# Performance work log

Hardware: AMD Instinct MI355X
Metric: run time of the kernel (lower is better)

## Reference

```python
import jax, jax.numpy as jnp
import numpy as np

NQ = 6      # configuration_dim = state_dim // 2
HID = 32    # hidden_dim
NL = 5      # num_layers


def _mlp(x, W0, b0, Wh, bh, Wo, bo):
    # Sequential: NL softplus hidden layers, then linear head
    h = jax.nn.softplus(x @ W0 + b0)
    for i in range(Wh.shape[0]):
        h = jax.nn.softplus(h @ Wh[i] + bh[i])
    return h @ Wo + bo


def _make_mlp_params(key, din, dout):
    k0, k1, k2 = jax.random.split(key, 3)
    s = lambda fan: 1.0 / np.sqrt(fan)
    return (jax.random.normal(k0, (din, HID), jnp.float32) * s(din),
            jnp.zeros((HID,), jnp.float32),
            jax.random.normal(k1, (NL - 1, HID, HID), jnp.float32) * s(HID),
            jnp.zeros((NL - 1, HID), jnp.float32),
            jax.random.normal(k2, (HID, dout), jnp.float32) * s(HID),
            jnp.zeros((dout,), jnp.float32))


def setup_inputs() -> dict:
    key = jax.random.key(0)
    kx, km, ku, kd, ka = jax.random.split(key, 5)
    B, input_dim = 65536, 6
    inputs = jax.random.normal(kx, (B, 2 * NQ + input_dim), jnp.float32)
    m = _make_mlp_params(km, NQ, NQ * NQ)   # mass matrix net
    u = _make_mlp_params(ku, NQ, 1)          # potential energy net
    d = _make_mlp_params(kd, NQ, NQ * NQ)   # damping matrix net
    A = jax.random.normal(ka, (input_dim, NQ), jnp.float32) / np.sqrt(input_dim)
    out = {"inputs": inputs, "A": A}
    names = ["W0", "b0", "Wh", "bh", "Wo", "bo"]
    for pfx, ps in (("m", m), ("u", u), ("d", d)):
        for n, p in zip(names, ps):
            out[pfx + "_" + n] = p
    return out


def reference(inputs, A,
              m_W0, m_b0, m_Wh, m_bh, m_Wo, m_bo,
              u_W0, u_b0, u_Wh, u_bh, u_Wo, u_bo,
              d_W0, d_b0, d_Wh, d_bh, d_Wo, d_bo):
    nq = NQ
    y, tau = inputs[:, :2 * nq], inputs[:, 2 * nq:]
    x, xd = y[:, :nq], y[:, nq:]

    # learned dissipation: tau_d = D(x) @ x_d (batched)
    D = _mlp(x, d_W0, d_b0, d_Wh, d_bh, d_Wo, d_bo).reshape(-1, nq, nq)
    tau_d = jnp.einsum('bij,bj->bi', D, xd)

    # learned input matrix: Dense(nq, use_bias=False)
    tau_ext = tau @ A

    def potential(q):
        return _mlp(q, u_W0, u_b0, u_Wh, u_bh, u_Wo, u_bo).sum()

    def kinetic(q, qd):
        M = _mlp(q, m_W0, m_b0, m_Wh, m_bh, m_Wo, m_bo).reshape(nq, nq)
        return 0.5 * qd @ (M @ qd)

    def dyn(q, qd, t_ext, t_d):
        tau_pot = jax.grad(potential)(q)
        H = jax.hessian(kinetic, argnums=(0, 1))(q, qd)
        d2L_dq_dqd = H[1][0]   # d/dq of dT/dqd  -> Coriolis term matrix
        M = H[1][1]            # d2T/dqd2 = 0.5*(M_nn + M_nn^T)
        tau_cor = d2L_dq_dqd @ qd
        return jnp.linalg.inv(M) @ (t_ext - tau_cor - tau_pot - t_d)

    return jax.vmap(dyn)(x, xd, tau_ext, tau_d)
```

## Files before the change

kernel.cpp:

```cpp
#include <hip/hip_runtime.h>


#define NQ 6
#define HID 32
#define NHID 4

#define MW0T 0
#define UW0T 192
#define DW0T 384
#define MWHT 576
#define UWHT (576 + 4096)
#define DWHT (576 + 8192)
#define MWOT (576 + 12288)
#define DWOT (MWOT + 1152)
#define UWOT (DWOT + 1152)
#define W0P_M 15200
#define W0P_U 15488
#define W0P_D 15744
#define WSYM 16000
#define BSYM 16672
#define SC_BASE 16896

#define L_W0P 0
#define L_WHT 256
#define LM_WSYM 4864
#define LM_BSYM 5620
#define LM_B0 5644
#define LM_BH 5676
#define LM_HT 5804
#define LM_XD 10668
#define LM_TC 11052
#define LM_TOT 11440
#define LU_WHO 4864
#define LU_WO 9472
#define LU_W0O 9504
#define LU_B0 9720
#define LU_BH 9752
#define LU_S 9880
#define LU_HB 19096
#define LU_HD 28312
#define LU_TOT 37528
#define LD_WOT 4864
#define LD_B0 6160
#define LD_BH 6192
#define LD_BO 6320
#define LD_S 6356
#define LD_TOT 10964

__device__ const int IU21[21] = {0, 0, 0, 0, 0, 0, 1, 1, 1, 1, 1, 2, 2, 2, 2, 3, 3, 3, 4, 4, 5};
__device__ const int JU21[21] = {0, 1, 2, 3, 4, 5, 1, 2, 3, 4, 5, 2, 3, 4, 5, 3, 4, 5, 4, 5, 5};

__global__ void prep_kernel(const float* __restrict__ mW0, const float* __restrict__ mWh,
                            const float* __restrict__ mWo, const float* __restrict__ m_bo,
                            const float* __restrict__ uW0, const float* __restrict__ uWh,
                            const float* __restrict__ uWo, const float* __restrict__ dW0,
                            const float* __restrict__ dWh, const float* __restrict__ dWo,
                            float* __restrict__ ws) {
  int t = blockIdx.x * blockDim.x + threadIdx.x;
  if (t < 192) {
    int j = t / 6, k = t % 6;
    ws[MW0T + t] = mW0[k * HID + j];
    ws[UW0T + t] = uW0[k * HID + j];
    ws[DW0T + t] = dW0[k * HID + j];
  }
  if (t < 256) {
    int j = t >> 3, k = t & 7;
    float vm = 0.f, vu = 0.f, vd = 0.f;
    if (k < 6) {
      vm = mW0[k * HID + j];
      vu = uW0[k * HID + j];
      vd = dW0[k * HID + j];
    }
    ws[W0P_M + t] = vm;
    ws[W0P_U + t] = vu;
    ws[W0P_D + t] = vd;
  }
  if (t < 4096) {
    int l = t >> 10, j = (t >> 5) & 31, k = t & 31;
    int src = l * 1024 + k * 32 + j;
    ws[MWHT + t] = mWh[src];
    ws[UWHT + t] = uWh[src];
    ws[DWHT + t] = dWh[src];
  }
  if (t < 1152) {
    int o = t / 32, k = t % 32;
    ws[MWOT + t] = mWo[k * 36 + o];
    ws[DWOT + t] = dWo[k * 36 + o];
  }
  if (t < 32) ws[UWOT + t] = uWo[t];
  if (t < 672) {
    int p = t >> 5, k = t & 31;
    int i = IU21[p], j = JU21[p];
    ws[WSYM + t] = 0.5f * (mWo[k * 36 + i * 6 + j] + mWo[k * 36 + j * 6 + i]);
  }
  if (t < 21) {
    int i = IU21[t], j = JU21[t];
    ws[BSYM + t] = 0.5f * (m_bo[i * 6 + j] + m_bo[j * 6 + i]);
  }
}

__device__ __forceinline__ float sp1(float z) {
  return fmaxf(z, 0.f) + __logf(1.f + __expf(-fabsf(z)));
}
__device__ __forceinline__ void sp_sig(float z, float& hs, float& sg) {
  float e = __expf(-fabsf(z));
  float d = __builtin_amdgcn_rcpf(1.f + e);
  hs = fmaxf(z, 0.f) + __logf(1.f + e);
  sg = (z >= 0.f ? 1.f : e) * d;
}
__device__ __forceinline__ float sig_h(float h) { return 1.f - __expf(-h); }

__device__ __forceinline__ void cpy4n(float* __restrict__ dst, const float* __restrict__ src,
                                      int n4, int t, int nt) {
  const float4* s = (const float4*)src;
  float4* d = (float4*)dst;
  for (int i = t; i < n4; i += nt) d[i] = s[i];
}
__device__ __forceinline__ void cpysn(float* __restrict__ dst, const float* __restrict__ src,
                                      int n, int t, int nt) {
  for (int i = t; i < n; i += nt) dst[i] = src[i];
}
__device__ __forceinline__ void stage36n(float* __restrict__ dst, const float* __restrict__ src,
                                         int nrows, int t, int nt) {
  int n4 = nrows * 8;
  for (int i = t; i < n4; i += nt) {
    int r = i >> 3, c = i & 7;
    *(float4*)&dst[r * 36 + c * 4] = *(const float4*)&src[r * 32 + c * 4];
  }
}

__device__ __forceinline__ void load32(const float* p, float* hv) {
#pragma unroll
  for (int c = 0; c < 8; c++) {
    float4 v = *(const float4*)&p[4 * c];
    hv[4 * c + 0] = v.x;
    hv[4 * c + 1] = v.y;
    hv[4 * c + 2] = v.z;
    hv[4 * c + 3] = v.w;
  }
}
__device__ __forceinline__ void load64(const float* p, float* hv) {
#pragma unroll
  for (int c = 0; c < 16; c++) {
    float4 v = *(const float4*)&p[4 * c];
    hv[4 * c + 0] = v.x;
    hv[4 * c + 1] = v.y;
    hv[4 * c + 2] = v.z;
    hv[4 * c + 3] = v.w;
  }
}
__device__ __forceinline__ float dot32(const float* hv, const float* r) {
  float s = 0.f;
#pragma unroll
  for (int c = 0; c < 8; c++) {
    float4 w = *(const float4*)&r[4 * c];
    s += hv[4 * c + 0] * w.x + hv[4 * c + 1] * w.y + hv[4 * c + 2] * w.z + hv[4 * c + 3] * w.w;
  }
  return s;
}
__device__ __forceinline__ float2 dotP(const float* hv2, const float* r, float bias) {
  float ax = bias, ay = 0.f;
#pragma unroll
  for (int c = 0; c < 8; c++) {
    float4 w = *(const float4*)&r[4 * c];
    ax += w.x * hv2[8 * c + 0];
    ay += w.x * hv2[8 * c + 1];
    ax += w.y * hv2[8 * c + 2];
    ay += w.y * hv2[8 * c + 3];
    ax += w.z * hv2[8 * c + 4];
    ay += w.z * hv2[8 * c + 5];
    ax += w.w * hv2[8 * c + 6];
    ay += w.w * hv2[8 * c + 7];
  }
  return make_float2(ax, ay);
}

__device__ __forceinline__ void coopFwd2(const float* Wb, const float* bh, const float* s0,
                                         const float* s1, float* d0, float* d1, int q) {
  float a0[32], a1[32];
  load32(s0, a0);
  load32(s1, a1);
#pragma unroll 2
  for (int m8 = 0; m8 < 8; m8++) {
    int j = q + 4 * m8;
    const float* r = Wb + j * 36;
    float z0 = bh[j], z1 = bh[j];
#pragma unroll
    for (int c = 0; c < 8; c++) {
      float4 w = *(const float4*)&r[4 * c];
      z0 += a0[4 * c + 0] * w.x + a0[4 * c + 1] * w.y + a0[4 * c + 2] * w.z + a0[4 * c + 3] * w.w;
      z1 += a1[4 * c + 0] * w.x + a1[4 * c + 1] * w.y + a1[4 * c + 2] * w.z + a1[4 * c + 3] * w.w;
    }
    d0[j] = sp1(z0);
    d1[j] = sp1(z1);
  }
}
__device__ __forceinline__ void coopFwd2O(const float* Wb, const float* bh, const float* s0,
                                          const float* s1, float* d0, float* d1, int o) {
  float a0[32], a1[32];
  load32(s0, a0);
  load32(s1, a1);
#pragma unroll
  for (int m4 = 0; m4 < 4; m4++) {
    int j = o + 8 * m4;
    const float* r = Wb + j * 36;
    float z0 = bh[j], z1 = bh[j];
#pragma unroll
    for (int c = 0; c < 8; c++) {
      float4 w = *(const float4*)&r[4 * c];
      z0 += a0[4 * c + 0] * w.x + a0[4 * c + 1] * w.y + a0[4 * c + 2] * w.z + a0[4 * c + 3] * w.w;
      z1 += a1[4 * c + 0] * w.x + a1[4 * c + 1] * w.y + a1[4 * c + 2] * w.z + a1[4 * c + 3] * w.w;
    }
    d0[j] = sp1(z0);
    d1[j] = sp1(z1);
  }
}
__device__ __forceinline__ void coopBwd2O(const float* Wb, const float* s0, const float* s1,
                                          float* d0, float* d1, int o) {
  float a0[32], a1[32];
  load32(s0, a0);
  load32(s1, a1);
#pragma unroll
  for (int m4 = 0; m4 < 4; m4++) {
    int k = o + 8 * m4;
    const float* r = Wb + k * 36;
    float z0 = 0.f, z1 = 0.f;
#pragma unroll
    for (int c = 0; c < 8; c++) {
      float4 w = *(const float4*)&r[4 * c];
      z0 += a0[4 * c + 0] * w.x + a0[4 * c + 1] * w.y + a0[4 * c + 2] * w.z + a0[4 * c + 3] * w.w;
      z1 += a1[4 * c + 0] * w.x + a1[4 * c + 1] * w.y + a1[4 * c + 2] * w.z + a1[4 * c + 3] * w.w;
    }
    d0[k] = z0;
    d1[k] = z1;
  }
}
__device__ __forceinline__ void coopFusedP(const float* Wb, const float* bh, float* ht, int o) {
  float hv[64];
  load64(ht, hv);
#pragma unroll
  for (int m4 = 0; m4 < 4; m4++) {
    int j = o + 8 * m4;
    float2 z = dotP(hv, Wb + j * 36, bh[j]);
    float hs, sg;
    sp_sig(z.x, hs, sg);
    *(float2*)&ht[2 * j] = make_float2(hs, z.y * sg);
  }
}

__global__ __launch_bounds__(512, 1) void mrole_kernel(const float* __restrict__ in,
                                                       const float* __restrict__ ws,
                                                       const float* __restrict__ m_b0,
                                                       const float* __restrict__ m_bh,
                                                       float* __restrict__ sc, int B) {
  __shared__ __align__(16) float L[LM_TOT];
  __shared__ int PIJ[21];
  const int t = threadIdx.x;
  cpy4n(L + L_W0P, ws + W0P_M, 64, t, 512);
  stage36n(L + L_WHT, ws + MWHT, 128, t, 512);
  stage36n(L + LM_WSYM, ws + WSYM, 21, t, 512);
  cpysn(L + LM_BSYM, ws + BSYM, 21, t, 512);
  cpysn(L + LM_B0, m_b0, 32, t, 512);
  cpysn(L + LM_BH, m_bh, 128, t, 512);
  if (t < 21) PIJ[t] = (IU21[t] << 3) | JU21[t];
  __syncthreads();

  const int el = t >> 3, o = t & 7;
  const int e = blockIdx.x * 64 + el;
  if (e >= B) return;
  const float* ip = in + (long)e * 18;
  const long Bl = B;

  float x0 = ip[0], x1 = ip[1], x2 = ip[2], x3 = ip[3], x4 = ip[4], x5 = ip[5];
  float d0 = ip[6], d1 = ip[7], d2 = ip[8], d3 = ip[9], d4 = ip[10], d5 = ip[11];
  if (o < 6) {
    L[LM_XD + el * 6 + o] = ip[6 + o];
    L[LM_TC + el * 6 + o] = 0.f;
  }
  float* ht = L + LM_HT + el * 76;
#pragma unroll
  for (int m4 = 0; m4 < 4; m4++) {
    int j = o + 8 * m4;
    float4 wa = *(const float4*)&L[L_W0P + j * 8];
    float4 wb = *(const float4*)&L[L_W0P + j * 8 + 4];
    float zh = L[LM_B0 + j] + x0 * wa.x + x1 * wa.y + x2 * wa.z + x3 * wa.w + x4 * wb.x + x5 * wb.y;
    float zt = d0 * wa.x + d1 * wa.y + d2 * wa.z + d3 * wa.w + d4 * wb.x + d5 * wb.y;
    float hs, sg;
    sp_sig(zh, hs, sg);
    *(float2*)&ht[2 * j] = make_float2(hs, zt * sg);
  }
#pragma unroll 1
  for (int l = 0; l < 4; l++) coopFusedP(L + L_WHT + l * 1152, L + LM_BH + l * 32, ht, o);
  float hv[64];
  load64(ht, hv);
#pragma unroll 1
  for (int mm = 0; mm < 3; mm++) {
    int p = o + 8 * mm;
    if (p < 21) {
      float2 vw = dotP(hv, L + LM_WSYM + p * 36, L[LM_BSYM + p]);
      sc[(long)p * Bl + e] = vw.x;
      int pij = PIJ[p];
      int iu = pij >> 3, ju = pij & 7;
      float xdj = L[LM_XD + el * 6 + ju];
      atomicAdd(&L[LM_TC + el * 6 + iu], vw.y * xdj);
      if (iu != ju) {
        float xdi = L[LM_XD + el * 6 + iu];
        atomicAdd(&L[LM_TC + el * 6 + ju], vw.y * xdi);
      }
    }
  }
  if (o < 6) sc[(long)(21 + o) * Bl + e] = L[LM_TC + el * 6 + o];
}

__global__ __launch_bounds__(1024, 1) void urole_kernel(
    const float* __restrict__ in, const float* __restrict__ ws, const float* __restrict__ u_W0,
    const float* __restrict__ u_b0, const float* __restrict__ u_Wh, const float* __restrict__ u_bh,
    const float* __restrict__ u_Wo, float* __restrict__ sc, int B) {
  __shared__ __align__(16) float L[LU_TOT];
  const int t = threadIdx.x;
  cpy4n(L + L_W0P, ws + W0P_U, 64, t, 1024);
  stage36n(L + L_WHT, ws + UWHT, 128, t, 1024);
  stage36n(L + LU_WHO, u_Wh, 128, t, 1024);
  cpy4n(L + LU_WO, u_Wo, 8, t, 1024);
  stage36n(L + LU_W0O, u_W0, 6, t, 1024);
  cpysn(L + LU_B0, u_b0, 32, t, 1024);
  cpysn(L + LU_BH, u_bh, 128, t, 1024);
  __syncthreads();

  const int oid = t >> 3, o = t & 7;
  const int e0 = blockIdx.x * 256 + oid;
  if (e0 >= B) return;
  const int e1 = e0 + 128;
  const bool has1 = e1 < B;
  const int el0 = oid, el1 = oid + 128;
  const float* ip0 = in + (long)e0 * 18;
  const float* ip1 = in + (long)(has1 ? e1 : e0) * 18;
  const long Bl = B;

  float X0[6], X1[6];
#pragma unroll
  for (int i = 0; i < 6; i++) {
    X0[i] = ip0[i];
    X1[i] = ip1[i];
  }
  float* S0 = L + LU_S + el0 * 36;
  float* S1 = L + LU_S + el1 * 36;
  float* HB0 = L + LU_HB + el0 * 36;
  float* HB1 = L + LU_HB + el1 * 36;
  float* HD0 = L + LU_HD + el0 * 36;
  float* HD1 = L + LU_HD + el1 * 36;
#pragma unroll
  for (int m4 = 0; m4 < 4; m4++) {
    int j = o + 8 * m4;
    float4 wa = *(const float4*)&L[L_W0P + j * 8];
    float4 wb = *(const float4*)&L[L_W0P + j * 8 + 4];
    float b = L[LU_B0 + j];
    S0[j] = sp1(b + X0[0] * wa.x + X0[1] * wa.y + X0[2] * wa.z + X0[3] * wa.w + X0[4] * wb.x +
                X0[5] * wb.y);
    S1[j] = sp1(b + X1[0] * wa.x + X1[1] * wa.y + X1[2] * wa.z + X1[3] * wa.w + X1[4] * wb.x +
                X1[5] * wb.y);
  }
  coopFwd2O(L + L_WHT + 0 * 1152, L + LU_BH + 0, S0, S1, HB0, HB1, o);
  coopFwd2O(L + L_WHT + 1 * 1152, L + LU_BH + 32, HB0, HB1, S0, S1, o);
  coopFwd2O(L + L_WHT + 2 * 1152, L + LU_BH + 64, S0, S1, HD0, HD1, o);
  coopFwd2O(L + L_WHT + 3 * 1152, L + LU_BH + 96, HD0, HD1, S0, S1, o);
#pragma unroll
  for (int m4 = 0; m4 < 4; m4++) {
    int j = o + 8 * m4;
    float wo = L[LU_WO + j];
    S0[j] = wo * sig_h(S0[j]);
    S1[j] = wo * sig_h(S1[j]);
  }
  coopBwd2O(L + LU_WHO + 3 * 1152, S0, S1, S0, S1, o);
#pragma unroll
  for (int m4 = 0; m4 < 4; m4++) {
    int j = o + 8 * m4;
    S0[j] = S0[j] * sig_h(HD0[j]);
    S1[j] = S1[j] * sig_h(HD1[j]);
  }
  coopBwd2O(L + LU_WHO + 2 * 1152, S0, S1, HD0, HD1, o);
  coopFwd2O(L + L_WHT + 1 * 1152, L + LU_BH + 32, HB0, HB1, S0, S1, o);
#pragma unroll
  for (int m4 = 0; m4 < 4; m4++) {
    int j = o + 8 * m4;
    HD0[j] = HD0[j] * sig_h(S0[j]);
    HD1[j] = HD1[j] * sig_h(S1[j]);
  }
  coopBwd2O(L + LU_WHO + 1 * 1152, HD0, HD1, S0, S1, o);
#pragma unroll
  for (int m4 = 0; m4 < 4; m4++) {
    int j = o + 8 * m4;
    HB0[j] = S0[j] * sig_h(HB0[j]);
    HB1[j] = S1[j] * sig_h(HB1[j]);
  }
  coopBwd2O(L + LU_WHO + 0 * 1152, HB0, HB1, HD0, HD1, o);
#pragma unroll
  for (int m4 = 0; m4 < 4; m4++) {
    int j = o + 8 * m4;
    float4 wa = *(const float4*)&L[L_W0P + j * 8];
    float4 wb = *(const float4*)&L[L_W0P + j * 8 + 4];
    float b = L[LU_B0 + j];
    float a0 = sp1(b + X0[0] * wa.x + X0[1] * wa.y + X0[2] * wa.z + X0[3] * wa.w + X0[4] * wb.x +
                   X0[5] * wb.y);
    float a1 = sp1(b + X1[0] * wa.x + X1[1] * wa.y + X1[2] * wa.z + X1[3] * wa.w + X1[4] * wb.x +
                   X1[5] * wb.y);
    S0[j] = HD0[j] * sig_h(a0);
    S1[j] = HD1[j] * sig_h(a1);
  }
  if (o < 6) {
    float a0[32], a1[32];
    load32(S0, a0);
    load32(S1, a1);
    const float* r = L + LU_W0O + o * 36;
    float tp0 = 0.f, tp1 = 0.f;
#pragma unroll
    for (int c = 0; c < 8; c++) {
      float4 w = *(const float4*)&r[4 * c];
      tp0 += a0[4 * c + 0] * w.x + a0[4 * c + 1] * w.y + a0[4 * c + 2] * w.z + a0[4 * c + 3] * w.w;
      tp1 += a1[4 * c + 0] * w.x + a1[4 * c + 1] * w.y + a1[4 * c + 2] * w.z + a1[4 * c + 3] * w.w;
    }
    sc[(long)(27 + o) * Bl + e0] = tp0;
    if (has1) sc[(long)(27 + o) * Bl + e1] = tp1;
  }
}

__global__ __launch_bounds__(256, 1) void drole_kernel(const float* __restrict__ in,
                                                       const float* __restrict__ ws,
                                                       const float* __restrict__ d_b0,
                                                       const float* __restrict__ d_bh,
                                                       const float* __restrict__ d_bo,
                                                       float* __restrict__ sc, int B) {
  __shared__ __align__(16) float L[LD_TOT];
  const int t = threadIdx.x;
  cpy4n(L + L_W0P, ws + W0P_D, 64, t, 256);
  stage36n(L + L_WHT, ws + DWHT, 128, t, 256);
  stage36n(L + LD_WOT, ws + DWOT, 36, t, 256);
  cpysn(L + LD_B0, d_b0, 32, t, 256);
  cpysn(L + LD_BH, d_bh, 128, t, 256);
  cpysn(L + LD_BO, d_bo, 36, t, 256);
  __syncthreads();

  const int qid = t >> 2, q = t & 3;
  const int e0 = blockIdx.x * 128 + qid;
  if (e0 >= B) return;
  const int e1 = e0 + 64;
  const bool has1 = e1 < B;
  const int el0 = qid, el1 = qid + 64;
  const float* ip0 = in + (long)e0 * 18;
  const float* ip1 = in + (long)(has1 ? e1 : e0) * 18;
  const long Bl = B;

  float X0[6], X1[6];
#pragma unroll
  for (int i = 0; i < 6; i++) {
    X0[i] = ip0[i];
    X1[i] = ip1[i];
  }
  float* S0 = L + LD_S + el0 * 36;
  float* S1 = L + LD_S + el1 * 36;
#pragma unroll 2
  for (int m8 = 0; m8 < 8; m8++) {
    int j = q + 4 * m8;
    float4 wa = *(const float4*)&L[L_W0P + j * 8];
    float4 wb = *(const float4*)&L[L_W0P + j * 8 + 4];
    float b = L[LD_B0 + j];
    S0[j] = sp1(b + X0[0] * wa.x + X0[1] * wa.y + X0[2] * wa.z + X0[3] * wa.w + X0[4] * wb.x +
                X0[5] * wb.y);
    S1[j] = sp1(b + X1[0] * wa.x + X1[1] * wa.y + X1[2] * wa.z + X1[3] * wa.w + X1[4] * wb.x +
                X1[5] * wb.y);
  }
#pragma unroll 1
  for (int l = 0; l < 4; l++)
    coopFwd2(L + L_WHT + l * 1152, L + LD_BH + l * 32, S0, S1, S0, S1, q);
  float a0[32], a1[32];
  load32(S0, a0);
  load32(S1, a1);
#pragma unroll 1
  for (int mm = 0; mm < 2; mm++) {
    int i = q + 4 * mm;
    if (i < 6) {
      float td0 = 0.f, td1 = 0.f;
#pragma unroll 1
      for (int c = 0; c < 6; c++) {
        const float* r = L + LD_WOT + (i * 6 + c) * 36;
        float b = L[LD_BO + i * 6 + c];
        float v0 = b, v1 = b;
#pragma unroll
        for (int cc = 0; cc < 8; cc++) {
          float4 w = *(const float4*)&r[4 * cc];
          v0 += a0[4 * cc + 0] * w.x + a0[4 * cc + 1] * w.y + a0[4 * cc + 2] * w.z +
                a0[4 * cc + 3] * w.w;
          v1 += a1[4 * cc + 0] * w.x + a1[4 * cc + 1] * w.y + a1[4 * cc + 2] * w.z +
                a1[4 * cc + 3] * w.w;
        }
        td0 += v0 * ip0[6 + c];
        td1 += v1 * ip1[6 + c];
      }
      sc[(long)(33 + i) * Bl + e0] = td0;
      if (has1) sc[(long)(33 + i) * Bl + e1] = td1;
    }
  }
}

__global__ __launch_bounds__(256) void combine_kernel(const float* __restrict__ in,
                                                      const float* __restrict__ A,
                                                      const float* __restrict__ sc,
                                                      float* __restrict__ out, int B) {
  int b = blockIdx.x * 256 + threadIdx.x;
  if (b >= B) return;
  const long Bl = B;
  const float* ip = in + (long)b * 18;
  float te[6];
  {
    float tv[6];
#pragma unroll
    for (int i = 0; i < 6; i++) tv[i] = ip[12 + i];
#pragma unroll
    for (int i = 0; i < 6; i++) {
      float s = 0.f;
#pragma unroll
      for (int j = 0; j < 6; j++) s += tv[j] * A[j * 6 + i];
      te[i] = s;
    }
  }
  float Ms[6][6], r[6], y[6];
  {
    int idx = 0;
#pragma unroll
    for (int i = 0; i < 6; i++)
#pragma unroll
      for (int j = i; j < 6; j++) {
        float v = sc[idx * Bl + b];
        Ms[i][j] = v;
        Ms[j][i] = v;
        idx++;
      }
  }
#pragma unroll
  for (int i = 0; i < 6; i++)
    r[i] = te[i] - sc[(21 + i) * Bl + b] - sc[(27 + i) * Bl + b] - sc[(33 + i) * Bl + b];

#pragma unroll
  for (int k = 0; k < 6; k++) {
#pragma unroll
    for (int rr = k + 1; rr < 6; rr++) {
      bool c = fabsf(Ms[rr][k]) > fabsf(Ms[k][k]);
#pragma unroll
      for (int j = 0; j < 6; j++) {
        float a = Ms[k][j], bb = Ms[rr][j];
        Ms[k][j] = c ? bb : a;
        Ms[rr][j] = c ? a : bb;
      }
      float a = r[k], bb = r[rr];
      r[k] = c ? bb : a;
      r[rr] = c ? a : bb;
    }
    float piv = Ms[k][k];
#pragma unroll
    for (int rr = k + 1; rr < 6; rr++) {
      float f = Ms[rr][k] / piv;
#pragma unroll
      for (int j = k; j < 6; j++) Ms[rr][j] -= f * Ms[k][j];
      r[rr] -= f * r[k];
    }
  }
#pragma unroll
  for (int ki = 5; ki >= 0; ki--) {
    float v = r[ki];
#pragma unroll
    for (int j = ki + 1; j < 6; j++) v -= Ms[ki][j] * y[j];
    y[ki] = v / Ms[ki][ki];
  }
  float* op = out + (long)b * 6;
#pragma unroll
  for (int i = 0; i < 6; i++) op[i] = y[i];
}

__device__ __forceinline__ void fwd_layer(const float* __restrict__ Wb,
                                          const float* __restrict__ bh,
                                          const float* __restrict__ hin, float* __restrict__ hout) {
#pragma unroll
  for (int j = 0; j < 32; j++) {
    const float* r = Wb + j * 32;
    float z = bh[j];
#pragma unroll
    for (int k = 0; k < 32; k++) z += hin[k] * r[k];
    hout[j] = sp1(z);
  }
}
__device__ __forceinline__ void m_layer(const float* __restrict__ Wb, const float* __restrict__ bh,
                                        float* __restrict__ h, const float* __restrict__ tin,
                                        float* __restrict__ tout) {
#pragma unroll
  for (int j = 0; j < 32; j++) {
    const float* r = Wb + j * 32;
    float z = bh[j];
#pragma unroll
    for (int k = 0; k < 32; k++) z += h[k] * r[k];
    tout[j] = z;
  }
#pragma unroll
  for (int j = 0; j < 32; j++) {
    const float* r = Wb + j * 32;
    float z = 0.f;
#pragma unroll
    for (int k = 0; k < 32; k++) z += tin[k] * r[k];
    float hs, sg;
    sp_sig(tout[j], hs, sg);
    h[j] = hs;
    tout[j] = z * sg;
  }
}
__device__ __forceinline__ void bwd_mv(const float* __restrict__ Worig,
                                       const float* __restrict__ gin, float* __restrict__ gout) {
#pragma unroll
  for (int k = 0; k < 32; k++) {
    const float* r = Worig + k * 32;
    float s = 0.f;
#pragma unroll
    for (int j = 0; j < 32; j++) s += r[j] * gin[j];
    gout[k] = s;
  }
}

__global__ __launch_bounds__(64, 1) void lnn_kernel(
    const float* __restrict__ in, const float* __restrict__ A, const float* __restrict__ ws,
    const float* __restrict__ m_b0, const float* __restrict__ m_bh, const float* __restrict__ m_bo,
    const float* __restrict__ u_W0, const float* __restrict__ u_b0, const float* __restrict__ u_Wh,
    const float* __restrict__ u_bh, const float* __restrict__ u_Wo,
    const float* __restrict__ d_b0, const float* __restrict__ d_bh, const float* __restrict__ d_bo,
    float* __restrict__ out, int B) {
  int b = blockIdx.x * 64 + threadIdx.x;
  if (b >= B) return;
  const float* ip = in + (long)b * 18;
  float x[6], xd[6], te[6];
#pragma unroll
  for (int i = 0; i < 6; i++) {
    x[i] = ip[i];
    xd[i] = ip[6 + i];
  }
  {
    float tv[6];
#pragma unroll
    for (int i = 0; i < 6; i++) tv[i] = ip[12 + i];
#pragma unroll
    for (int i = 0; i < 6; i++) {
      float s = 0.f;
#pragma unroll
      for (int j = 0; j < 6; j++) s += tv[j] * A[j * 6 + i];
      te[i] = s;
    }
  }
  float td[6] = {0, 0, 0, 0, 0, 0};
  {
    float h[32], zn[32];
    const float* w0 = ws + DW0T;
#pragma unroll
    for (int j = 0; j < 32; j++) {
      float z = d_b0[j];
#pragma unroll
      for (int k = 0; k < 6; k++) z += x[k] * w0[j * 6 + k];
      h[j] = sp1(z);
    }
    fwd_layer(ws + DWHT + 0 * 1024, d_bh + 0, h, zn);
    fwd_layer(ws + DWHT + 1 * 1024, d_bh + 32, zn, h);
    fwd_layer(ws + DWHT + 2 * 1024, d_bh + 64, h, zn);
    fwd_layer(ws + DWHT + 3 * 1024, d_bh + 96, zn, h);
    const float* wo = ws + DWOT;
#pragma unroll
    for (int o = 0; o < 36; o++) {
      float v = d_bo[o];
#pragma unroll
      for (int k = 0; k < 32; k++) v += h[k] * wo[o * 32 + k];
      td[o / 6] += v * xd[o % 6];
    }
  }
  float tp[6] = {0, 0, 0, 0, 0, 0};
  {
    float hb[32], hd[32], s[32], r2[32];
    const float* w0 = ws + UW0T;
#pragma unroll
    for (int j = 0; j < 32; j++) {
      float z = u_b0[j];
#pragma unroll
      for (int k = 0; k < 6; k++) z += x[k] * w0[j * 6 + k];
      s[j] = sp1(z);
    }
    fwd_layer(ws + UWHT + 0 * 1024, u_bh + 0, s, hb);
    fwd_layer(ws + UWHT + 1 * 1024, u_bh + 32, hb, s);
    fwd_layer(ws + UWHT + 2 * 1024, u_bh + 64, s, hd);
    fwd_layer(ws + UWHT + 3 * 1024, u_bh + 96, hd, s);
#pragma unroll
    for (int j = 0; j < 32; j++) s[j] = u_Wo[j] * sig_h(s[j]);
    bwd_mv(u_Wh + 3 * 1024, s, r2);
#pragma unroll
    for (int j = 0; j < 32; j++) s[j] = r2[j] * sig_h(hd[j]);
    bwd_mv(u_Wh + 2 * 1024, s, hd);
    fwd_layer(ws + UWHT + 1 * 1024, u_bh + 32, hb, s);
#pragma unroll
    for (int j = 0; j < 32; j++) r2[j] = hd[j] * sig_h(s[j]);
    bwd_mv(u_Wh + 1 * 1024, r2, s);
#pragma unroll
    for (int j = 0; j < 32; j++) r2[j] = s[j] * sig_h(hb[j]);
    bwd_mv(u_Wh + 0 * 1024, r2, hb);
#pragma unroll
    for (int j = 0; j < 32; j++) {
      float z = u_b0[j];
#pragma unroll
      for (int k = 0; k < 6; k++) z += x[k] * w0[j * 6 + k];
      s[j] = sp1(z);
    }
#pragma unroll
    for (int j = 0; j < 32; j++) s[j] = hb[j] * sig_h(s[j]);
#pragma unroll
    for (int i = 0; i < 6; i++) {
      float t = 0.f;
#pragma unroll
      for (int j = 0; j < 32; j++) t += u_W0[i * 32 + j] * s[j];
      tp[i] = t;
    }
  }
  float Ms[6][6], tc[6];
  {
    float h[32], t[32], zn[32];
    const float* w0 = ws + MW0T;
#pragma unroll
    for (int j = 0; j < 32; j++) {
      float zh = m_b0[j], zt = 0.f;
#pragma unroll
      for (int k = 0; k < 6; k++) {
        zh += x[k] * w0[j * 6 + k];
        zt += xd[k] * w0[j * 6 + k];
      }
      float hs, sg;
      sp_sig(zh, hs, sg);
      h[j] = hs;
      t[j] = zt * sg;
    }
    m_layer(ws + MWHT + 0 * 1024, m_bh + 0, h, t, zn);
    m_layer(ws + MWHT + 1 * 1024, m_bh + 32, h, zn, t);
    m_layer(ws + MWHT + 2 * 1024, m_bh + 64, h, t, zn);
    m_layer(ws + MWHT + 3 * 1024, m_bh + 96, h, zn, t);
    const float* wo = ws + MWOT;
    float Msv[21];
    int idx = 0;
#pragma unroll
    for (int i = 0; i < 6; i++) tc[i] = 0.f;
#pragma unroll
    for (int i = 0; i < 6; i++)
#pragma unroll
      for (int j = i; j < 6; j++) {
        const float* r = wo + (i * 6 + j) * 32;
        float v = m_bo[i * 6 + j], w = 0.f;
#pragma unroll
        for (int k = 0; k < 32; k++) {
          v += h[k] * r[k];
          w += t[k] * r[k];
        }
        if (i != j) {
          const float* rr = wo + (j * 6 + i) * 32;
          float v2 = m_bo[j * 6 + i], w2 = 0.f;
#pragma unroll
          for (int k = 0; k < 32; k++) {
            v2 += h[k] * rr[k];
            w2 += t[k] * rr[k];
          }
          v = 0.5f * (v + v2);
          w = 0.5f * (w + w2);
        }
        Msv[idx] = v;
        tc[i] += w * xd[j];
        if (j != i) tc[j] += w * xd[i];
        idx++;
      }
    idx = 0;
#pragma unroll
    for (int i = 0; i < 6; i++)
#pragma unroll
      for (int j = i; j < 6; j++) {
        Ms[i][j] = Msv[idx];
        Ms[j][i] = Msv[idx];
        idx++;
      }
  }
  float r[6], y[6];
#pragma unroll
  for (int i = 0; i < 6; i++) r[i] = te[i] - tc[i] - tp[i] - td[i];
#pragma unroll
  for (int k = 0; k < 6; k++) {
#pragma unroll
    for (int rr = k + 1; rr < 6; rr++) {
      bool c = fabsf(Ms[rr][k]) > fabsf(Ms[k][k]);
#pragma unroll
      for (int j = 0; j < 6; j++) {
        float a = Ms[k][j], bb = Ms[rr][j];
        Ms[k][j] = c ? bb : a;
        Ms[rr][j] = c ? a : bb;
      }
      float a = r[k], bb = r[rr];
      r[k] = c ? bb : a;
      r[rr] = c ? a : bb;
    }
    float piv = Ms[k][k];
#pragma unroll
    for (int rr = k + 1; rr < 6; rr++) {
      float f = Ms[rr][k] / piv;
#pragma unroll
      for (int j = k; j < 6; j++) Ms[rr][j] -= f * Ms[k][j];
      r[rr] -= f * r[k];
    }
  }
#pragma unroll
  for (int ki = 5; ki >= 0; ki--) {
    float v = r[ki];
#pragma unroll
    for (int j = ki + 1; j < 6; j++) v -= Ms[ki][j] * y[j];
    y[ki] = v / Ms[ki][ki];
  }
  float* op = out + (long)b * 6;
#pragma unroll
  for (int i = 0; i < 6; i++) op[i] = y[i];
}

extern "C" void kernel_launch(void* const* d_in, const int* in_sizes, int n_in, void* d_out,
                              int out_size, void* d_ws, size_t ws_size, hipStream_t stream) {
  const float* inputs = (const float*)d_in[0];
  const float* A = (const float*)d_in[1];
  const float* m_W0 = (const float*)d_in[2];
  const float* m_b0 = (const float*)d_in[3];
  const float* m_Wh = (const float*)d_in[4];
  const float* m_bh = (const float*)d_in[5];
  const float* m_Wo = (const float*)d_in[6];
  const float* m_bo = (const float*)d_in[7];
  const float* u_W0 = (const float*)d_in[8];
  const float* u_b0 = (const float*)d_in[9];
  const float* u_Wh = (const float*)d_in[10];
  const float* u_bh = (const float*)d_in[11];
  const float* u_Wo = (const float*)d_in[12];
  const float* d_W0 = (const float*)d_in[14];
  const float* d_b0 = (const float*)d_in[15];
  const float* d_Wh = (const float*)d_in[16];
  const float* d_bh = (const float*)d_in[17];
  const float* d_Wo = (const float*)d_in[18];
  const float* d_bo = (const float*)d_in[19];

  float* ws = (float*)d_ws;
  float* out = (float*)d_out;
  int B = in_sizes[0] / 18;

  prep_kernel<<<16, 256, 0, stream>>>(m_W0, m_Wh, m_Wo, m_bo, u_W0, u_Wh, u_Wo, d_W0, d_Wh, d_Wo,
                                      ws);

  size_t need = (size_t)(SC_BASE + (size_t)B * 39) * 4;
  if (ws_size >= need) {
    float* sc = ws + SC_BASE;
    int nb_m = (B + 63) / 64;
    int nb_d = (B + 127) / 128;
    int nb_u = (B + 255) / 256;
    mrole_kernel<<<nb_m, 512, 0, stream>>>(inputs, ws, m_b0, m_bh, sc, B);
    urole_kernel<<<nb_u, 1024, 0, stream>>>(inputs, ws, u_W0, u_b0, u_Wh, u_bh, u_Wo, sc, B);
    drole_kernel<<<nb_d, 256, 0, stream>>>(inputs, ws, d_b0, d_bh, d_bo, sc, B);
    combine_kernel<<<(B + 255) / 256, 256, 0, stream>>>(inputs, A, sc, out, B);
  } else {
    lnn_kernel<<<(B + 63) / 64, 64, 0, stream>>>(inputs, A, ws, m_b0, m_bh, m_bo, u_W0, u_b0, u_Wh,
                                                 u_bh, u_Wo, d_b0, d_bh, d_bo, out, B);
  }
}
```

Measured before the change: 109.3 us.

## Map two threads per element in mass-matrix kernel instead of eight

The mass-net kernel now assigns each batch element to 2 threads instead of 8. Each block covers 256 elements instead of 64, and the per-element shared scratch grows to match. Each thread computes 16 hidden units per layer and up to 11 symmetric outputs. The goal is to amortise the per-thread load of the 64-value hidden/tangent vector over more outputs, reduce redundant LDS traffic, and amortise weight staging over more elements per block. The trade-off is fewer, larger blocks with heavier shared-memory use, which lowers occupancy and thread-level parallelism for this stage.

```diff
diff --git a/kernel.cpp b/kernel.cpp
--- a/kernel.cpp
+++ b/kernel.cpp
@@ -28,9 +28,9 @@
 #define LM_B0 5644
 #define LM_BH 5676
 #define LM_HT 5804
-#define LM_XD 10668
-#define LM_TC 11052
-#define LM_TOT 11440
+#define LM_XD 25260
+#define LM_TC 26796
+#define LM_TOT 28336
 #define LU_WHO 4864
 #define LU_WO 9472
 #define LU_W0O 9504
@@ -149,15 +149,6 @@
     hv[4 * c + 3] = v.w;
   }
 }
-__device__ __forceinline__ float dot32(const float* hv, const float* r) {
-  float s = 0.f;
-#pragma unroll
-  for (int c = 0; c < 8; c++) {
-    float4 w = *(const float4*)&r[4 * c];
-    s += hv[4 * c + 0] * w.x + hv[4 * c + 1] * w.y + hv[4 * c + 2] * w.z + hv[4 * c + 3] * w.w;
-  }
-  return s;
-}
 __device__ __forceinline__ float2 dotP(const float* hv2, const float* r, float bias) {
   float ax = bias, ay = 0.f;
 #pragma unroll
@@ -235,12 +226,12 @@
     d1[k] = z1;
   }
 }
-__device__ __forceinline__ void coopFusedP(const float* Wb, const float* bh, float* ht, int o) {
+__device__ __forceinline__ void coopFusedP2(const float* Wb, const float* bh, float* ht, int o) {
   float hv[64];
   load64(ht, hv);
-#pragma unroll
-  for (int m4 = 0; m4 < 4; m4++) {
-    int j = o + 8 * m4;
+#pragma unroll 2
+  for (int m16 = 0; m16 < 16; m16++) {
+    int j = o + 2 * m16;
     float2 z = dotP(hv, Wb + j * 36, bh[j]);
     float hs, sg;
     sp_sig(z.x, hs, sg);
@@ -265,22 +256,24 @@
   if (t < 21) PIJ[t] = (IU21[t] << 3) | JU21[t];
   __syncthreads();
 
-  const int el = t >> 3, o = t & 7;
-  const int e = blockIdx.x * 64 + el;
+  const int el = t >> 1, o = t & 1;
+  const int e = blockIdx.x * 256 + el;
   if (e >= B) return;
   const float* ip = in + (long)e * 18;
   const long Bl = B;
 
   float x0 = ip[0], x1 = ip[1], x2 = ip[2], x3 = ip[3], x4 = ip[4], x5 = ip[5];
   float d0 = ip[6], d1 = ip[7], d2 = ip[8], d3 = ip[9], d4 = ip[10], d5 = ip[11];
-  if (o < 6) {
-    L[LM_XD + el * 6 + o] = ip[6 + o];
-    L[LM_TC + el * 6 + o] = 0.f;
-  }
+  L[LM_XD + el * 6 + o] = ip[6 + o];
+  L[LM_XD + el * 6 + o + 2] = ip[8 + o];
+  L[LM_XD + el * 6 + o + 4] = ip[10 + o];
+  L[LM_TC + el * 6 + o] = 0.f;
+  L[LM_TC + el * 6 + o + 2] = 0.f;
+  L[LM_TC + el * 6 + o + 4] = 0.f;
   float* ht = L + LM_HT + el * 76;
-#pragma unroll
-  for (int m4 = 0; m4 < 4; m4++) {
-    int j = o + 8 * m4;
+#pragma unroll 2
+  for (int m16 = 0; m16 < 16; m16++) {
+    int j = o + 2 * m16;
     float4 wa = *(const float4*)&L[L_W0P + j * 8];
     float4 wb = *(const float4*)&L[L_W0P + j * 8 + 4];
     float zh = L[LM_B0 + j] + x0 * wa.x + x1 * wa.y + x2 * wa.z + x3 * wa.w + x4 * wb.x + x5 * wb.y;
@@ -290,12 +283,12 @@
     *(float2*)&ht[2 * j] = make_float2(hs, zt * sg);
   }
 #pragma unroll 1
-  for (int l = 0; l < 4; l++) coopFusedP(L + L_WHT + l * 1152, L + LM_BH + l * 32, ht, o);
+  for (int l = 0; l < 4; l++) coopFusedP2(L + L_WHT + l * 1152, L + LM_BH + l * 32, ht, o);
   float hv[64];
   load64(ht, hv);
 #pragma unroll 1
-  for (int mm = 0; mm < 3; mm++) {
-    int p = o + 8 * mm;
+  for (int mm = 0; mm < 11; mm++) {
+    int p = o + 2 * mm;
     if (p < 21) {
       float2 vw = dotP(hv, L + LM_WSYM + p * 36, L[LM_BSYM + p]);
       sc[(long)p * Bl + e] = vw.x;
@@ -309,7 +302,9 @@
       }
     }
   }
-  if (o < 6) sc[(long)(21 + o) * Bl + e] = L[LM_TC + el * 6 + o];
+  sc[(long)(21 + o) * Bl + e] = L[LM_TC + el * 6 + o];
+  sc[(long)(23 + o) * Bl + e] = L[LM_TC + el * 6 + o + 2];
+  sc[(long)(25 + o) * Bl + e] = L[LM_TC + el * 6 + o + 4];
 }
 
 __global__ __launch_bounds__(1024, 1) void urole_kernel(
@@ -854,7 +849,7 @@
   size_t need = (size_t)(SC_BASE + (size_t)B * 39) * 4;
   if (ws_size >= need) {
     float* sc = ws + SC_BASE;
-    int nb_m = (B + 63) / 64;
+    int nb_m = (B + 255) / 256;
     int nb_d = (B + 127) / 128;
     int nb_u = (B + 255) / 256;
     mrole_kernel<<<nb_m, 512, 0, stream>>>(inputs, ws, m_b0, m_bh, sc, B);
```

Measured after the change: 107.1 us, median of 2. 1.02x faster.
